# Kernel optimization log

Measured on AMD Instinct MI355X. Metric: run time of the kernel, lower is better.

## Reference

```python
import jax, jax.numpy as jnp
import numpy as np

N_NODES = 50000
N_EDGES = 800000
D_FEAT = 96
HOP_NUM = 4


def setup_inputs() -> dict:
    key = jax.random.key(0)
    k1, k2, k3, k4, k5 = jax.random.split(key, 5)
    h = jax.random.normal(k1, (N_NODES, D_FEAT), dtype=jnp.float32)
    # per-node degree-normalization scalar (ndata['d']), e.g. deg^{-1/2}
    d = jax.random.uniform(k2, (N_NODES,), dtype=jnp.float32)
    src = jax.random.randint(k3, (N_EDGES,), 0, N_NODES)
    dst = jax.random.randint(k4, (N_EDGES,), 0, N_NODES)
    # layerRegular: hop_num learned scalars, init U[0,1)
    layer_regular = jax.random.uniform(k5, (HOP_NUM,), dtype=jnp.float32)
    return {"h": h, "d": d, "src": src, "dst": dst, "layer_regular": layer_regular}


def reference(h, d, src, dst, layer_regular):
    # edge weights: e = d_dst * d_src  (edge_applying with m == 1)
    e = (d[dst] * d[src])[:, None]  # [E, 1]

    def spmm(x):
        # update_all(u_mul_e('h','e'), sum): gather src feats, scale, scatter-add to dst
        return jax.ops.segment_sum(x[src] * e, dst, num_segments=N_NODES)

    feat = h
    hops = []
    for i in range(HOP_NUM):
        r = layer_regular[i]
        feat = spmm(feat) * r + (1.0 - r) * feat  # residual blend
        # feature_drop with p=0.0 is identity
        hops.append(feat)
    return jnp.concatenate(hops, axis=1)  # [N, hop_num * D]
```

## Files before the change

kernel.cpp:

```cpp
#include <hip/hip_runtime.h>

#define N_NODES 50000
#define N_EDGES 800000
#define D_FEAT 96
#define HOP_NUM 4
#define OUT_STRIDE (HOP_NUM * D_FEAT)
#define SCAN_B 256
#define NBLK_SCAN ((N_NODES + SCAN_B - 1) / SCAN_B)

struct Edge { int s; float w; };

__device__ __forceinline__ unsigned short f2bf(float x) {
    union { float f; unsigned u; } c; c.f = x;
    unsigned r = (c.u + 0x7FFFu + ((c.u >> 16) & 1u)) >> 16;
    return (unsigned short)r;
}
__device__ __forceinline__ float bf2f(unsigned short b) {
    union { unsigned u; float f; } c; c.u = ((unsigned)b) << 16;
    return c.f;
}


__global__ void zero_deg_kernel(int* __restrict__ deg) {
    int i = blockIdx.x * blockDim.x + threadIdx.x;
    if (i < N_NODES) deg[i] = 0;
}

__global__ void hist_kernel(const int* __restrict__ dst, int* __restrict__ deg) {
    int e = blockIdx.x * blockDim.x + threadIdx.x;
    if (e >= N_EDGES) return;
    atomicAdd(&deg[dst[e]], 1);
}

__global__ void scanA_kernel(const int* __restrict__ deg, int* __restrict__ off,
                             int* __restrict__ partials) {
    int i = blockIdx.x * SCAN_B + threadIdx.x;
    int v = (i < N_NODES) ? deg[i] : 0;
    int lane = threadIdx.x & 63;
    int wid  = threadIdx.x >> 6;
    int x = v;
    #pragma unroll
    for (int o = 1; o < 64; o <<= 1) {
        int y = __shfl_up(x, o, 64);
        if (lane >= o) x += y;
    }
    __shared__ int wtot[SCAN_B / 64];
    if (lane == 63) wtot[wid] = x;
    __syncthreads();
    int wbase = 0;
    #pragma unroll
    for (int w = 0; w < SCAN_B / 64; ++w) wbase += (w < wid) ? wtot[w] : 0;
    if (i < N_NODES) off[i] = wbase + x - v;
    if (threadIdx.x == SCAN_B - 1) partials[blockIdx.x] = wbase + x;
}

__global__ void scanB_kernel(int* __restrict__ partials) {
    int tid = threadIdx.x;
    int v = (tid < NBLK_SCAN) ? partials[tid] : 0;
    int lane = tid & 63;
    int wid  = tid >> 6;
    int x = v;
    #pragma unroll
    for (int o = 1; o < 64; o <<= 1) {
        int y = __shfl_up(x, o, 64);
        if (lane >= o) x += y;
    }
    __shared__ int wtot[SCAN_B / 64];
    if (lane == 63) wtot[wid] = x;
    __syncthreads();
    int wbase = 0;
    #pragma unroll
    for (int w = 0; w < SCAN_B / 64; ++w) wbase += (w < wid) ? wtot[w] : 0;
    if (tid < NBLK_SCAN) partials[tid] = wbase + x - v;
}

__global__ void scanC_kernel(int* __restrict__ off, const int* __restrict__ partials,
                             int* __restrict__ cursor) {
    int i = blockIdx.x * SCAN_B + threadIdx.x;
    if (i < N_NODES) {
        off[i] += partials[blockIdx.x];
        cursor[i] = 0;
    }
    if (i == 0) off[N_NODES] = N_EDGES;
}

__global__ void scatter_kernel(const int* __restrict__ src, const int* __restrict__ dst,
                               const float* __restrict__ dn,
                               const int* __restrict__ off, int* __restrict__ cursor,
                               Edge* __restrict__ edges) {
    int e = blockIdx.x * blockDim.x + threadIdx.x;
    if (e >= N_EDGES) return;
    int t = dst[e];
    int s = src[e];
    float w = dn[s] * dn[t];
    int p = atomicAdd(&cursor[t], 1);
    Edge ed; ed.s = s; ed.w = w;
    edges[off[t] + p] = ed;
}

__global__ void f32_to_bf16_kernel(const float* __restrict__ in, unsigned short* __restrict__ out) {
    int i = blockIdx.x * blockDim.x + threadIdx.x;
    if (i >= N_NODES * D_FEAT / 4) return;
    float4 v = ((const float4*)in)[i];
    ushort4 o;
    o.x = f2bf(v.x); o.y = f2bf(v.y); o.z = f2bf(v.z); o.w = f2bf(v.w);
    ((ushort4*)out)[i] = o;
}

__global__ void spmm_gather_kernel(const unsigned short* __restrict__ tab,
                                   const int* __restrict__ off,
                                   const Edge* __restrict__ edges,
                                   const float* __restrict__ lr, int hop,
                                   float* __restrict__ out,
                                   unsigned short* __restrict__ tab_next) {
    int gid = (blockIdx.x * blockDim.x + threadIdx.x) >> 5;
    int lane = threadIdx.x & 31;
    if (gid >= N_NODES) return;
    int beg = off[gid];
    int end = off[gid + 1];
    const bool ch = (lane < 24);

    float4 acc = make_float4(0.f, 0.f, 0.f, 0.f);
    for (int b = beg; b < end; b += 32) {
        int m = min(32, end - b);
        int s_l = 0; float w_l = 0.f;
        if (lane < m) {
            Edge ed = edges[b + lane];
            s_l = ed.s; w_l = ed.w;
        }
        int j = 0;
        for (; j + 4 <= m; j += 4) {
            int   s0 = __shfl(s_l, j,     32);
            int   s1 = __shfl(s_l, j + 1, 32);
            int   s2 = __shfl(s_l, j + 2, 32);
            int   s3 = __shfl(s_l, j + 3, 32);
            float w0 = __shfl(w_l, j,     32);
            float w1 = __shfl(w_l, j + 1, 32);
            float w2 = __shfl(w_l, j + 2, 32);
            float w3 = __shfl(w_l, j + 3, 32);
            if (ch) {
                ushort4 u0 = ((const ushort4*)(tab + (long long)s0 * D_FEAT))[lane];
                ushort4 u1 = ((const ushort4*)(tab + (long long)s1 * D_FEAT))[lane];
                ushort4 u2 = ((const ushort4*)(tab + (long long)s2 * D_FEAT))[lane];
                ushort4 u3 = ((const ushort4*)(tab + (long long)s3 * D_FEAT))[lane];
                acc.x = fmaf(bf2f(u0.x), w0, fmaf(bf2f(u1.x), w1, fmaf(bf2f(u2.x), w2, fmaf(bf2f(u3.x), w3, acc.x))));
                acc.y = fmaf(bf2f(u0.y), w0, fmaf(bf2f(u1.y), w1, fmaf(bf2f(u2.y), w2, fmaf(bf2f(u3.y), w3, acc.y))));
                acc.z = fmaf(bf2f(u0.z), w0, fmaf(bf2f(u1.z), w1, fmaf(bf2f(u2.z), w2, fmaf(bf2f(u3.z), w3, acc.z))));
                acc.w = fmaf(bf2f(u0.w), w0, fmaf(bf2f(u1.w), w1, fmaf(bf2f(u2.w), w2, fmaf(bf2f(u3.w), w3, acc.w))));
            }
        }
        for (; j < m; ++j) {
            int   s = __shfl(s_l, j, 32);
            float w = __shfl(w_l, j, 32);
            if (ch) {
                ushort4 u = ((const ushort4*)(tab + (long long)s * D_FEAT))[lane];
                acc.x = fmaf(bf2f(u.x), w, acc.x);
                acc.y = fmaf(bf2f(u.y), w, acc.y);
                acc.z = fmaf(bf2f(u.z), w, acc.z);
                acc.w = fmaf(bf2f(u.w), w, acc.w);
            }
        }
    }

    if (ch) {
        float r = lr[hop];
        ushort4 pu = ((const ushort4*)(tab + (long long)gid * D_FEAT))[lane];
        float4 o;
        o.x = acc.x * r + (1.0f - r) * bf2f(pu.x);
        o.y = acc.y * r + (1.0f - r) * bf2f(pu.y);
        o.z = acc.z * r + (1.0f - r) * bf2f(pu.z);
        o.w = acc.w * r + (1.0f - r) * bf2f(pu.w);
        ((float4*)(out + (long long)gid * OUT_STRIDE))[lane] = o;
        if (tab_next) {
            ushort4 ov;
            ov.x = f2bf(o.x); ov.y = f2bf(o.y); ov.z = f2bf(o.z); ov.w = f2bf(o.w);
            ((ushort4*)(tab_next + (long long)gid * D_FEAT))[lane] = ov;
        }
    }
}

extern "C" void kernel_launch(void* const* d_in, const int* in_sizes, int n_in,
                              void* d_out, int out_size, void* d_ws, size_t ws_size,
                              hipStream_t stream) {
    const float* h   = (const float*)d_in[0];
    const float* dn  = (const float*)d_in[1];
    const int*   src = (const int*)d_in[2];
    const int*   dst = (const int*)d_in[3];
    const float* lr  = (const float*)d_in[4];
    float* out = (float*)d_out;

    char* base = (char*)d_ws;
    Edge* edges = (Edge*)base;              base += (size_t)N_EDGES * sizeof(Edge);
    unsigned short* tabA = (unsigned short*)base; base += (size_t)N_NODES * D_FEAT * sizeof(unsigned short);
    unsigned short* tabB = (unsigned short*)base; base += (size_t)N_NODES * D_FEAT * sizeof(unsigned short);
    int* off      = (int*)base;             base += (N_NODES + 1) * sizeof(int);
    int* deg      = (int*)base;             base += N_NODES * sizeof(int);
    int* partials = (int*)base;             base += NBLK_SCAN * sizeof(int);

    const int EB = (N_EDGES + 255) / 256;

    zero_deg_kernel<<<NBLK_SCAN, SCAN_B, 0, stream>>>(deg);
    hist_kernel<<<EB, 256, 0, stream>>>(dst, deg);
    scanA_kernel<<<NBLK_SCAN, SCAN_B, 0, stream>>>(deg, off, partials);
    scanB_kernel<<<1, SCAN_B, 0, stream>>>(partials);
    scanC_kernel<<<NBLK_SCAN, SCAN_B, 0, stream>>>(off, partials, deg);
    scatter_kernel<<<EB, 256, 0, stream>>>(src, dst, dn, off, deg, edges);
    f32_to_bf16_kernel<<<(N_NODES * D_FEAT / 4 + 255) / 256, 256, 0, stream>>>(h, tabA);

    const int GROUPS_PER_BLOCK = 8;
    const int HB = (N_NODES + GROUPS_PER_BLOCK - 1) / GROUPS_PER_BLOCK;
    unsigned short* cur = tabA;
    unsigned short* nxt = tabB;
    for (int hop = 0; hop < HOP_NUM; ++hop) {
        unsigned short* wr = (hop == HOP_NUM - 1) ? (unsigned short*)nullptr : nxt;
        spmm_gather_kernel<<<HB, 256, 0, stream>>>(cur, off, edges, lr, hop,
                                                   out + hop * D_FEAT, wr);
        unsigned short* t = cur; cur = nxt; nxt = t;
    }
}
```

Baseline: 214.5 us.

## Drop scan fixup kernel, fuse scatter with bf16 conversion, nontemporal output stores

Removes the third scan pass. Block-local offsets stay in `off`, and the block prefix from `partials` is added at use time in the scatter and gather kernels. The edge scatter and the f32-to-bf16 conversion of `h` are merged into one launch whose blocks split by index range. Cursor zeroing moves into the first scan kernel. Output rows are written with nontemporal stores. The aim is fewer kernel launches and less cache pollution from the write-only output, at the cost of an extra `partials` lookup per node in every hop.

```diff
diff --git a/kernel.cpp b/kernel.cpp
--- a/kernel.cpp
+++ b/kernel.cpp
@@ -7,8 +7,12 @@
 #define OUT_STRIDE (HOP_NUM * D_FEAT)
 #define SCAN_B 256
 #define NBLK_SCAN ((N_NODES + SCAN_B - 1) / SCAN_B)
+#define EB_BLOCKS ((N_EDGES + 255) / 256)
+#define F2B_VEC (N_NODES * D_FEAT / 4)
+#define F2B_BLOCKS ((F2B_VEC + 255) / 256)
 
 struct Edge { int s; float w; };
+typedef float f32x4 __attribute__((ext_vector_type(4)));
 
 __device__ __forceinline__ unsigned short f2bf(float x) {
     union { float f; unsigned u; } c; c.f = x;
@@ -33,7 +37,7 @@
 }
 
 __global__ void scanA_kernel(const int* __restrict__ deg, int* __restrict__ off,
-                             int* __restrict__ partials) {
+                             int* __restrict__ partials, int* __restrict__ cursor) {
     int i = blockIdx.x * SCAN_B + threadIdx.x;
     int v = (i < N_NODES) ? deg[i] : 0;
     int lane = threadIdx.x & 63;
@@ -50,7 +54,11 @@
     int wbase = 0;
     #pragma unroll
     for (int w = 0; w < SCAN_B / 64; ++w) wbase += (w < wid) ? wtot[w] : 0;
-    if (i < N_NODES) off[i] = wbase + x - v;
+    if (i < N_NODES) {
+        off[i] = wbase + x - v;
+        cursor[i] = 0;
+    }
+    if (i == N_NODES - 1) off[N_NODES] = wbase + x;
     if (threadIdx.x == SCAN_B - 1) partials[blockIdx.x] = wbase + x;
 }
 
@@ -74,41 +82,35 @@
     if (tid < NBLK_SCAN) partials[tid] = wbase + x - v;
 }
 
-__global__ void scanC_kernel(int* __restrict__ off, const int* __restrict__ partials,
-                             int* __restrict__ cursor) {
-    int i = blockIdx.x * SCAN_B + threadIdx.x;
-    if (i < N_NODES) {
-        off[i] += partials[blockIdx.x];
-        cursor[i] = 0;
-    }
-    if (i == 0) off[N_NODES] = N_EDGES;
-}
-
-__global__ void scatter_kernel(const int* __restrict__ src, const int* __restrict__ dst,
-                               const float* __restrict__ dn,
-                               const int* __restrict__ off, int* __restrict__ cursor,
-                               Edge* __restrict__ edges) {
-    int e = blockIdx.x * blockDim.x + threadIdx.x;
-    if (e >= N_EDGES) return;
-    int t = dst[e];
-    int s = src[e];
-    float w = dn[s] * dn[t];
-    int p = atomicAdd(&cursor[t], 1);
-    Edge ed; ed.s = s; ed.w = w;
-    edges[off[t] + p] = ed;
-}
-
-__global__ void f32_to_bf16_kernel(const float* __restrict__ in, unsigned short* __restrict__ out) {
-    int i = blockIdx.x * blockDim.x + threadIdx.x;
-    if (i >= N_NODES * D_FEAT / 4) return;
-    float4 v = ((const float4*)in)[i];
-    ushort4 o;
-    o.x = f2bf(v.x); o.y = f2bf(v.y); o.z = f2bf(v.z); o.w = f2bf(v.w);
-    ((ushort4*)out)[i] = o;
+__global__ void scatter_f2bf_kernel(const int* __restrict__ src, const int* __restrict__ dst,
+                                    const float* __restrict__ dn,
+                                    const int* __restrict__ off, const int* __restrict__ partials,
+                                    int* __restrict__ cursor, Edge* __restrict__ edges,
+                                    const float* __restrict__ h, unsigned short* __restrict__ tab) {
+    int b = blockIdx.x;
+    if (b < EB_BLOCKS) {
+        int e = b * 256 + threadIdx.x;
+        if (e >= N_EDGES) return;
+        int t = dst[e];
+        int s = src[e];
+        float w = dn[s] * dn[t];
+        int p = atomicAdd(&cursor[t], 1);
+        int idx = off[t] + partials[t >> 8] + p;
+        Edge ed; ed.s = s; ed.w = w;
+        edges[idx] = ed;
+    } else {
+        int i = (b - EB_BLOCKS) * 256 + threadIdx.x;
+        if (i >= F2B_VEC) return;
+        float4 v = ((const float4*)h)[i];
+        ushort4 o;
+        o.x = f2bf(v.x); o.y = f2bf(v.y); o.z = f2bf(v.z); o.w = f2bf(v.w);
+        ((ushort4*)tab)[i] = o;
+    }
 }
 
 __global__ void spmm_gather_kernel(const unsigned short* __restrict__ tab,
                                    const int* __restrict__ off,
+                                   const int* __restrict__ partials,
                                    const Edge* __restrict__ edges,
                                    const float* __restrict__ lr, int hop,
                                    float* __restrict__ out,
@@ -116,8 +118,8 @@
     int gid = (blockIdx.x * blockDim.x + threadIdx.x) >> 5;
     int lane = threadIdx.x & 31;
     if (gid >= N_NODES) return;
-    int beg = off[gid];
-    int end = off[gid + 1];
+    int beg = off[gid] + partials[gid >> 8];
+    int end = off[gid + 1] + partials[(gid + 1) >> 8];
     const bool ch = (lane < 24);
 
     float4 acc = make_float4(0.f, 0.f, 0.f, 0.f);
@@ -165,12 +167,12 @@
     if (ch) {
         float r = lr[hop];
         ushort4 pu = ((const ushort4*)(tab + (long long)gid * D_FEAT))[lane];
-        float4 o;
+        f32x4 o;
         o.x = acc.x * r + (1.0f - r) * bf2f(pu.x);
         o.y = acc.y * r + (1.0f - r) * bf2f(pu.y);
         o.z = acc.z * r + (1.0f - r) * bf2f(pu.z);
         o.w = acc.w * r + (1.0f - r) * bf2f(pu.w);
-        ((float4*)(out + (long long)gid * OUT_STRIDE))[lane] = o;
+        __builtin_nontemporal_store(o, (f32x4*)(out + (long long)gid * OUT_STRIDE) + lane);
         if (tab_next) {
             ushort4 ov;
             ov.x = f2bf(o.x); ov.y = f2bf(o.y); ov.z = f2bf(o.z); ov.w = f2bf(o.w);
@@ -190,22 +192,20 @@
     float* out = (float*)d_out;
 
     char* base = (char*)d_ws;
-    Edge* edges = (Edge*)base;              base += (size_t)N_EDGES * sizeof(Edge);
+    Edge* edges = (Edge*)base;                    base += (size_t)N_EDGES * sizeof(Edge);
     unsigned short* tabA = (unsigned short*)base; base += (size_t)N_NODES * D_FEAT * sizeof(unsigned short);
     unsigned short* tabB = (unsigned short*)base; base += (size_t)N_NODES * D_FEAT * sizeof(unsigned short);
-    int* off      = (int*)base;             base += (N_NODES + 1) * sizeof(int);
-    int* deg      = (int*)base;             base += N_NODES * sizeof(int);
-    int* partials = (int*)base;             base += NBLK_SCAN * sizeof(int);
-
-    const int EB = (N_EDGES + 255) / 256;
+    int* off      = (int*)base;                   base += (N_NODES + 1) * sizeof(int);
+    int* deg      = (int*)base;                   base += N_NODES * sizeof(int);
+    int* cursor   = (int*)base;                   base += N_NODES * sizeof(int);
+    int* partials = (int*)base;                   base += NBLK_SCAN * sizeof(int);
 
     zero_deg_kernel<<<NBLK_SCAN, SCAN_B, 0, stream>>>(deg);
-    hist_kernel<<<EB, 256, 0, stream>>>(dst, deg);
-    scanA_kernel<<<NBLK_SCAN, SCAN_B, 0, stream>>>(deg, off, partials);
+    hist_kernel<<<EB_BLOCKS, 256, 0, stream>>>(dst, deg);
+    scanA_kernel<<<NBLK_SCAN, SCAN_B, 0, stream>>>(deg, off, partials, cursor);
     scanB_kernel<<<1, SCAN_B, 0, stream>>>(partials);
-    scanC_kernel<<<NBLK_SCAN, SCAN_B, 0, stream>>>(off, partials, deg);
-    scatter_kernel<<<EB, 256, 0, stream>>>(src, dst, dn, off, deg, edges);
-    f32_to_bf16_kernel<<<(N_NODES * D_FEAT / 4 + 255) / 256, 256, 0, stream>>>(h, tabA);
+    scatter_f2bf_kernel<<<EB_BLOCKS + F2B_BLOCKS, 256, 0, stream>>>(
+        src, dst, dn, off, partials, cursor, edges, h, tabA);
 
     const int GROUPS_PER_BLOCK = 8;
     const int HB = (N_NODES + GROUPS_PER_BLOCK - 1) / GROUPS_PER_BLOCK;
@@ -213,7 +213,7 @@
     unsigned short* nxt = tabB;
     for (int hop = 0; hop < HOP_NUM; ++hop) {
         unsigned short* wr = (hop == HOP_NUM - 1) ? (unsigned short*)nullptr : nxt;
-        spmm_gather_kernel<<<HB, 256, 0, stream>>>(cur, off, edges, lr, hop,
+        spmm_gather_kernel<<<HB, 256, 0, stream>>>(cur, off, partials, edges, lr, hop,
                                                    out + hop * D_FEAT, wr);
         unsigned short* t = cur; cur = nxt; nxt = t;
     }
```

Result: slower. 226.1 us (+5.4%).
